# Performance work log

Measured on AMD Instinct MI355X. Metric: run time of the kernel, lower is better.

Reference implementation:

```python
import jax, jax.numpy as jnp
import numpy as np

VOCAB, D, H, L, T1, B = 32000, 1024, 1024, 2, 513, 64


def setup_inputs() -> dict:
    key = jax.random.key(0)
    ks = jax.random.split(key, 6)
    s = 1.0 / np.sqrt(H)
    return {
        "tokens": jax.random.randint(ks[0], (T1, B), 0, VOCAB),
        "emb": jax.random.normal(ks[1], (VOCAB, D), jnp.float32),
        "W_ih": jax.random.normal(ks[2], (L, 4 * H, D), jnp.float32) * s,
        "W_hh": jax.random.normal(ks[3], (L, 4 * H, H), jnp.float32) * s,
        "b_ih": jax.random.normal(ks[4], (L, 4 * H), jnp.float32) * s,
        "b_hh": jax.random.normal(ks[5], (L, 4 * H), jnp.float32) * s,
    }


def _lstm_cell(x, h, c, W_ih_l, W_hh_l, b_ih_l, b_hh_l):
    # gates: [B, 4H]; PyTorch LSTMCell gate order: i, f, g, o
    gates = x @ W_ih_l.T + b_ih_l + h @ W_hh_l.T + b_hh_l
    i, f, g, o = jnp.split(gates, 4, axis=-1)
    c_new = jax.nn.sigmoid(f) * c + jax.nn.sigmoid(i) * jnp.tanh(g)
    h_new = jax.nn.sigmoid(o) * jnp.tanh(c_new)
    return h_new, c_new


def reference(tokens, emb, W_ih, W_hh, b_ih, b_hh):
    ids = tokens[:-1]                       # [T, B] per `input[:-1]`
    emb_tab = emb.at[0].set(0.0)            # padding_idx = PAD = 0
    x = emb_tab[ids]                        # [T, B, D]

    h0 = jnp.zeros((L, x.shape[1], H), x.dtype)
    c0 = jnp.zeros((L, x.shape[1], H), x.dtype)

    def step(carry, x_t):
        h, c = carry                        # each [L, B, H]
        inp = x_t
        hs, cs = [], []
        for l in range(L):                  # L is small & static
            h_l, c_l = _lstm_cell(inp, h[l], c[l], W_ih[l], W_hh[l], b_ih[l], b_hh[l])
            inp = h_l                       # dropout=0.0 (eval): identity
            hs.append(h_l)
            cs.append(c_l)
        return (jnp.stack(hs), jnp.stack(cs)), inp

    _, outputs = jax.lax.scan(step, (h0, c0), x)
    return outputs                          # [T, B, H]
```

## Files before the change

### kernel.cpp

```cpp
#include <hip/hip_runtime.h>

typedef _Float16 half_t;
typedef _Float16 half8 __attribute__((ext_vector_type(8)));
typedef float floatx4 __attribute__((ext_vector_type(4)));
typedef int int4v __attribute__((ext_vector_type(4)));
typedef unsigned uint4v __attribute__((ext_vector_type(4)));
typedef unsigned char uchar;

#define NSTEP 512
#define INV2048 (1.0f / 2048.0f)
#define NSLOT 64
#define SLOTE 65536

__device__ __forceinline__ uchar enc_e5m2(float x) {
  half_t h = (half_t)x;
  unsigned b = (unsigned)__builtin_bit_cast(unsigned short, h);
  return (uchar)(((b + 0x80u) >> 8) & 0xffu);
}

__device__ __forceinline__ half8 dec8(unsigned w0, unsigned w1) {
  uint4v u;
  u[0] = ((w0 & 0x000000ffu) << 8) | ((w0 & 0x0000ff00u) << 16);
  u[1] = ((w0 & 0x00ff0000u) >> 8) | (w0 & 0xff000000u);
  u[2] = ((w1 & 0x000000ffu) << 8) | ((w1 & 0x0000ff00u) << 16);
  u[3] = ((w1 & 0x00ff0000u) >> 8) | (w1 & 0xff000000u);
  return __builtin_bit_cast(half8, u);
}

__global__ void conv_w(const float* __restrict__ Wih, const float* __restrict__ Whh,
                       half_t* __restrict__ whi, uchar* __restrict__ wlo) {
  long e = (long)blockIdx.x * 256 + threadIdx.x;
  int i    = (int)(e & 7);
  int lane = (int)((e >> 3) & 63);
  int frag = (int)((e >> 9) & 15);
  int wv   = (int)((e >> 13) & 7);
  int wg   = (int)((e >> 16) & 127);
  int layer = (int)((e >> 23) & 1);
  int mt = frag & 1, kk = (frag >> 1) & 3, prt = frag >> 3;
  int mloc = mt * 16 + (lane & 15);
  int grow = (mloc >> 3) * 1024 + wg * 8 + (mloc & 7);
  int k = prt * 1024 + wv * 128 + kk * 32 + ((lane >> 4) * 8) + i;
  long base = ((long)layer << 22) + (long)grow * 1024;
  float v = (k < 1024) ? Wih[base + k] : Whh[base + (k - 1024)];
  half_t hi = (half_t)v;
  whi[e] = hi;
  wlo[e] = enc_e5m2((v - (float)hi) * 2048.0f);
}

__device__ __forceinline__ float sigm(float x) { return 1.f / (1.f + __expf(-x)); }
__device__ __forceinline__ float tanh_f(float x) {
  x = fminf(15.f, fmaxf(-15.f, x));
  float e = __expf(-2.f * x);
  return (1.f - e) / (1.f + e);
}

__device__ __forceinline__ void pollcnt(const int* base, int n, int lane) {
  const int* p0 = base + lane;
  const int* p1 = base + 64 + lane;
  for (;;) {
    int v0 = __hip_atomic_load(p0, __ATOMIC_RELAXED, __HIP_MEMORY_SCOPE_AGENT);
    int v1 = __hip_atomic_load(p1, __ATOMIC_RELAXED, __HIP_MEMORY_SCOPE_AGENT);
    if (__all((v0 >= n) && (v1 >= n))) break;
    __builtin_amdgcn_s_sleep(2);
  }
}

__launch_bounds__(512, 1)
__global__ void lstm_main(const int* __restrict__ tokens, const float* __restrict__ emb,
                          const float* __restrict__ bih, const float* __restrict__ bhh,
                          const half_t* __restrict__ whi, const uchar* __restrict__ wlo,
                          half_t* __restrict__ h1h, half_t* __restrict__ h2h,
                          int* __restrict__ fc, float* __restrict__ out) {
  __shared__ float part[8][32][68];
  __shared__ volatile int gate0, gate1;
  const int wgid = blockIdx.x;
  const int layer = wgid >> 7;
  const int wg = wgid & 127;
  const int tid = (int)threadIdx.x;
  const int wv = tid >> 6;
  const int lane = tid & 63;
  const int ln15 = lane & 15;
  const int kr = (lane >> 4) * 8;

  const int* f0 = fc;
  const int* f1 = fc + 1024;

  half8 whi_r[16];
  {
    const half_t* wb = whi + (((long)(layer * 128 + wg)) << 16) + wv * 8192;
    #pragma unroll
    for (int f = 0; f < 16; ++f)
      whi_r[f] = *(const half8*)(wb + f * 512 + lane * 8);
  }
  unsigned lw[16][2];
  {
    const uchar* lobw = wlo + (((long)(layer * 128 + wg)) << 16) + wv * 8192;
    #pragma unroll
    for (int f = 0; f < 16; ++f) {
      const unsigned* l = (const unsigned*)(lobw + (f << 9) + lane * 8);
      lw[f][0] = l[0]; lw[f][1] = l[1];
    }
  }

  float bsum[4];
  {
    int u = tid & 7;
    for (int g = 0; g < 4; ++g) {
      int bi = layer * 4096 + g * 1024 + wg * 8 + u;
      bsum[g] = bih[bi] + bhh[bi];
    }
  }
  float c = 0.f;
  if (tid == 0) { gate0 = 0; gate1 = 0; }
  __syncthreads();

  for (int t = 0; t < NSTEP; ++t) {
    if (layer == 0) {
      if (wv == 0 && t > 0) {
        pollcnt(f0, t, lane);
        if (t >= 49) pollcnt(f1, t - 48, lane);
        if (lane == 0) gate1 = t;
      }
    } else {
      if (wv == 0) {
        pollcnt(f0, t + 1, lane);
        if (lane == 0) gate0 = t + 1;
      } else if (wv == 1 && t > 0) {
        pollcnt(f1, t, lane);
        if (lane == 0) gate1 = t;
      }
    }

    floatx4 zero = {0.f, 0.f, 0.f, 0.f};
    floatx4 acc_h[2][4], acc_l[2][4];
    for (int a = 0; a < 2; ++a)
      for (int b = 0; b < 4; ++b) { acc_h[a][b] = zero; acc_l[a][b] = zero; }

    if (layer == 0) {
      int tk[4]; const float* rowp[4]; float msk[4];
      #pragma unroll
      for (int nt = 0; nt < 4; ++nt) {
        tk[nt] = tokens[t * 64 + nt * 16 + ln15];
        rowp[nt] = emb + (long)tk[nt] * 1024;
        msk[nt] = (tk[nt] == 0) ? 0.f : 1.f;
      }
      floatx4 bx0[2][4], bx1[2][4];
      {
        int kb = wv * 128 + kr;
        #pragma unroll
        for (int nt = 0; nt < 4; ++nt) {
          bx0[0][nt] = *(const floatx4*)(rowp[nt] + kb);
          bx1[0][nt] = *(const floatx4*)(rowp[nt] + kb + 4);
        }
      }
      #pragma unroll
      for (int kk = 0; kk < 4; ++kk) {
        const int cb = kk & 1, nx = cb ^ 1;
        if (kk < 3) {
          int kb = wv * 128 + (kk + 1) * 32 + kr;
          #pragma unroll
          for (int nt = 0; nt < 4; ++nt) {
            bx0[nx][nt] = *(const floatx4*)(rowp[nt] + kb);
            bx1[nx][nt] = *(const floatx4*)(rowp[nt] + kb + 4);
          }
        }
        half8 ah0 = whi_r[kk * 2];
        half8 ah1 = whi_r[kk * 2 + 1];
        half8 al0 = dec8(lw[kk * 2][0], lw[kk * 2][1]);
        half8 al1 = dec8(lw[kk * 2 + 1][0], lw[kk * 2 + 1][1]);
        #pragma unroll
        for (int nt = 0; nt < 4; ++nt) {
          half8 bh;
          #pragma unroll
          for (int q = 0; q < 4; ++q) {
            bh[q]     = (half_t)(bx0[cb][nt][q] * msk[nt]);
            bh[q + 4] = (half_t)(bx1[cb][nt][q] * msk[nt]);
          }
          acc_h[0][nt] = __builtin_amdgcn_mfma_f32_16x16x32_f16(ah0, bh, acc_h[0][nt], 0, 0, 0);
          acc_h[1][nt] = __builtin_amdgcn_mfma_f32_16x16x32_f16(ah1, bh, acc_h[1][nt], 0, 0, 0);
          acc_l[0][nt] = __builtin_amdgcn_mfma_f32_16x16x32_f16(al0, bh, acc_l[0][nt], 0, 0, 0);
          acc_l[1][nt] = __builtin_amdgcn_mfma_f32_16x16x32_f16(al1, bh, acc_l[1][nt], 0, 0, 0);
        }
      }
    } else {
      while (gate0 < t + 1) __builtin_amdgcn_s_sleep(1);
      const half_t* abh = h1h + (long)(t & (NSLOT - 1)) * SLOTE;
      const int kofs = wv * 128;
      half8 bufh[4][4];
      #pragma unroll
      for (int kk = 0; kk < 4; ++kk) {
        int kb = kofs + kk * 32 + kr;
        #pragma unroll
        for (int nt = 0; nt < 4; ++nt)
          bufh[kk][nt] = *(const half8*)(abh + (nt * 16 + ln15) * 1024 + kb);
      }
      #pragma unroll
      for (int kk = 0; kk < 4; ++kk) {
        half8 ah0 = whi_r[kk * 2];
        half8 ah1 = whi_r[kk * 2 + 1];
        half8 al0 = dec8(lw[kk * 2][0], lw[kk * 2][1]);
        half8 al1 = dec8(lw[kk * 2 + 1][0], lw[kk * 2 + 1][1]);
        #pragma unroll
        for (int nt = 0; nt < 4; ++nt) {
          half8 bh = bufh[kk][nt];
          acc_h[0][nt] = __builtin_amdgcn_mfma_f32_16x16x32_f16(ah0, bh, acc_h[0][nt], 0, 0, 0);
          acc_h[1][nt] = __builtin_amdgcn_mfma_f32_16x16x32_f16(ah1, bh, acc_h[1][nt], 0, 0, 0);
          acc_l[0][nt] = __builtin_amdgcn_mfma_f32_16x16x32_f16(al0, bh, acc_l[0][nt], 0, 0, 0);
          acc_l[1][nt] = __builtin_amdgcn_mfma_f32_16x16x32_f16(al1, bh, acc_l[1][nt], 0, 0, 0);
        }
      }
    }

    if (t > 0) {
      while (gate1 < t) __builtin_amdgcn_s_sleep(1);
      const half_t* abh = (layer == 0 ? h1h : h2h) + (long)((t - 1) & (NSLOT - 1)) * SLOTE;
      const int kofs = wv * 128;
      half8 bufh[4][4];
      #pragma unroll
      for (int kk = 0; kk < 4; ++kk) {
        int kb = kofs + kk * 32 + kr;
        #pragma unroll
        for (int nt = 0; nt < 4; ++nt)
          bufh[kk][nt] = *(const half8*)(abh + (nt * 16 + ln15) * 1024 + kb);
      }
      #pragma unroll
      for (int kk = 0; kk < 4; ++kk) {
        half8 ah0 = whi_r[8 + kk * 2];
        half8 ah1 = whi_r[8 + kk * 2 + 1];
        half8 al0 = dec8(lw[8 + kk * 2][0], lw[8 + kk * 2][1]);
        half8 al1 = dec8(lw[8 + kk * 2 + 1][0], lw[8 + kk * 2 + 1][1]);
        #pragma unroll
        for (int nt = 0; nt < 4; ++nt) {
          half8 bh = bufh[kk][nt];
          acc_h[0][nt] = __builtin_amdgcn_mfma_f32_16x16x32_f16(ah0, bh, acc_h[0][nt], 0, 0, 0);
          acc_h[1][nt] = __builtin_amdgcn_mfma_f32_16x16x32_f16(ah1, bh, acc_h[1][nt], 0, 0, 0);
          acc_l[0][nt] = __builtin_amdgcn_mfma_f32_16x16x32_f16(al0, bh, acc_l[0][nt], 0, 0, 0);
          acc_l[1][nt] = __builtin_amdgcn_mfma_f32_16x16x32_f16(al1, bh, acc_l[1][nt], 0, 0, 0);
        }
      }
    }

    #pragma unroll
    for (int mt = 0; mt < 2; ++mt)
      #pragma unroll
      for (int nt = 0; nt < 4; ++nt)
        #pragma unroll
        for (int q = 0; q < 4; ++q)
          part[wv][mt * 16 + (lane >> 4) * 4 + q][nt * 16 + ln15] =
              acc_h[mt][nt][q] + INV2048 * acc_l[mt][nt][q];
    __syncthreads();
    float hkeep;
    {
      int u = tid & 7, n = tid >> 3;
      float s0 = bsum[0], s1 = bsum[1], s2 = bsum[2], s3 = bsum[3];
      #pragma unroll
      for (int w = 0; w < 8; ++w) {
        s0 += part[w][u][n];
        s1 += part[w][8 + u][n];
        s2 += part[w][16 + u][n];
        s3 += part[w][24 + u][n];
      }
      float is = sigm(s0), fs = sigm(s1), gt = tanh_f(s2), os = sigm(s3);
      c = fs * c + is * gt;
      hkeep = os * tanh_f(c);
      half_t hhi = (half_t)hkeep;
      half_t* hb = (layer == 0 ? h1h : h2h) + (long)(t & (NSLOT - 1)) * SLOTE;
      __hip_atomic_store((unsigned short*)&hb[n * 1024 + wg * 8 + u],
                         __builtin_bit_cast(unsigned short, hhi),
                         __ATOMIC_RELAXED, __HIP_MEMORY_SCOPE_AGENT);
    }
    __syncthreads();
    if (tid == 0) {
      asm volatile("s_waitcnt vmcnt(0)" ::: "memory");
      __hip_atomic_store(fc + layer * 1024 + wg, t + 1,
                         __ATOMIC_RELAXED, __HIP_MEMORY_SCOPE_AGENT);
    }
    if (layer == 1) {
      int u = tid & 7, n = tid >> 3;
      __builtin_nontemporal_store(hkeep, &out[((long)t * 64 + n) * 1024 + wg * 8 + u]);
    }
    if ((t & 31) == 31)
      __builtin_amdgcn_fence(__ATOMIC_ACQUIRE, "agent");
  }
}

extern "C" void kernel_launch(void* const* d_in, const int* in_sizes, int n_in,
                              void* d_out, int out_size, void* d_ws, size_t ws_size,
                              hipStream_t stream) {
  const int*   tokens = (const int*)d_in[0];
  const float* emb    = (const float*)d_in[1];
  const float* Wih    = (const float*)d_in[2];
  const float* Whh    = (const float*)d_in[3];
  const float* bih    = (const float*)d_in[4];
  const float* bhh    = (const float*)d_in[5];
  float* out = (float*)d_out;

  half_t* whi = (half_t*)d_ws;
  uchar*  wlo = (uchar*)((char*)d_ws + 33554432);
  half_t* h1h = (half_t*)((char*)d_ws + 50331648);
  half_t* h2h = (half_t*)((char*)d_ws + 58720256);
  int* fc     = (int*)((char*)d_ws + 67108864);

  hipLaunchKernelGGL(conv_w, dim3(65536), dim3(256), 0, stream, Wih, Whh, whi, wlo);
  hipMemsetAsync(fc, 0, 8192, stream);

  void* args[] = {(void*)&tokens, (void*)&emb, (void*)&bih, (void*)&bhh,
                  (void*)&whi, (void*)&wlo, (void*)&h1h, (void*)&h2h,
                  (void*)&fc, (void*)&out};
  hipError_t e = hipLaunchCooperativeKernel((const void*)lstm_main, dim3(256), dim3(512),
                                            args, 0, stream);
  if (e != hipSuccess) {
    hipMemsetAsync(d_out, 0x43, (size_t)out_size * 4, stream);
  }
}
```

Measured before the change: 7.843 ms.

## Decentralize per-wave flag polling, pad flags, double-buffer partials and drop a barrier

Each wave now polls only the 16 producer flags covering its own K slice instead of wave 0 polling every flag and releasing the block through LDS gates. Flags are padded to separate 256-byte lines. The partial-sum LDS buffer is double-buffered, which lets the trailing __syncthreads be replaced by an LDS atomic counter whose last arriving wave publishes the completion flag. The aim is to cut the inter-workgroup synchronization latency on the recurrent critical path. In exchange, ordering now rests on per-wave waitcnt and relaxed atomics, and the layer-1 backpressure check on layer 0 runs only every 16 steps.

```diff
diff --git a/kernel.cpp b/kernel.cpp
--- a/kernel.cpp
+++ b/kernel.cpp
@@ -11,6 +11,7 @@
 #define INV2048 (1.0f / 2048.0f)
 #define NSLOT 64
 #define SLOTE 65536
+#define FSTRIDE 64
 
 __device__ __forceinline__ uchar enc_e5m2(float x) {
   half_t h = (half_t)x;
@@ -54,9 +55,15 @@
   return (1.f - e) / (1.f + e);
 }
 
-__device__ __forceinline__ void pollcnt(const int* base, int n, int lane) {
-  const int* p0 = base + lane;
-  const int* p1 = base + 64 + lane;
+__device__ __forceinline__ void pollN(const int* fbase, int first, int n, int lane) {
+  const int* p = fbase + (first + (lane & 15)) * FSTRIDE;
+  while (__hip_atomic_load(p, __ATOMIC_RELAXED, __HIP_MEMORY_SCOPE_AGENT) < n)
+    __builtin_amdgcn_s_sleep(2);
+}
+
+__device__ __forceinline__ void pollFull(const int* fbase, int n, int lane) {
+  const int* p0 = fbase + lane * FSTRIDE;
+  const int* p1 = fbase + (64 + lane) * FSTRIDE;
   for (;;) {
     int v0 = __hip_atomic_load(p0, __ATOMIC_RELAXED, __HIP_MEMORY_SCOPE_AGENT);
     int v1 = __hip_atomic_load(p1, __ATOMIC_RELAXED, __HIP_MEMORY_SCOPE_AGENT);
@@ -71,8 +78,8 @@
                           const half_t* __restrict__ whi, const uchar* __restrict__ wlo,
                           half_t* __restrict__ h1h, half_t* __restrict__ h2h,
                           int* __restrict__ fc, float* __restrict__ out) {
-  __shared__ float part[8][32][68];
-  __shared__ volatile int gate0, gate1;
+  __shared__ float part[2][8][32][68];
+  __shared__ int dcnt;
   const int wgid = blockIdx.x;
   const int layer = wgid >> 7;
   const int wg = wgid & 127;
@@ -83,7 +90,7 @@
   const int kr = (lane >> 4) * 8;
 
   const int* f0 = fc;
-  const int* f1 = fc + 1024;
+  const int* f1 = fc + 128 * FSTRIDE;
 
   half8 whi_r[16];
   {
@@ -111,24 +118,19 @@
     }
   }
   float c = 0.f;
-  if (tid == 0) { gate0 = 0; gate1 = 0; }
+  if (tid == 0) dcnt = 0;
   __syncthreads();
 
   for (int t = 0; t < NSTEP; ++t) {
     if (layer == 0) {
-      if (wv == 0 && t > 0) {
-        pollcnt(f0, t, lane);
-        if (t >= 49) pollcnt(f1, t - 48, lane);
-        if (lane == 0) gate1 = t;
-      }
+      if ((t & 15) == 0 && t >= 33) pollFull(f1, t - 32, lane);
+      if (t > 0) pollN(f0, wv * 16, t, lane);
     } else {
-      if (wv == 0) {
-        pollcnt(f0, t + 1, lane);
-        if (lane == 0) gate0 = t + 1;
-      } else if (wv == 1 && t > 0) {
-        pollcnt(f1, t, lane);
-        if (lane == 0) gate1 = t;
-      }
+      const int sel = (lane >> 4) & 1;
+      const int* p = (sel ? f0 : f1) + (wv * 16 + ln15) * FSTRIDE;
+      const int thr = sel ? (t + 1) : t;
+      while (__hip_atomic_load(p, __ATOMIC_RELAXED, __HIP_MEMORY_SCOPE_AGENT) < thr)
+        __builtin_amdgcn_s_sleep(2);
     }
 
     floatx4 zero = {0.f, 0.f, 0.f, 0.f};
@@ -183,7 +185,6 @@
         }
       }
     } else {
-      while (gate0 < t + 1) __builtin_amdgcn_s_sleep(1);
       const half_t* abh = h1h + (long)(t & (NSLOT - 1)) * SLOTE;
       const int kofs = wv * 128;
       half8 bufh[4][4];
@@ -212,7 +213,6 @@
     }
 
     if (t > 0) {
-      while (gate1 < t) __builtin_amdgcn_s_sleep(1);
       const half_t* abh = (layer == 0 ? h1h : h2h) + (long)((t - 1) & (NSLOT - 1)) * SLOTE;
       const int kofs = wv * 128;
       half8 bufh[4][4];
@@ -240,13 +240,14 @@
       }
     }
 
+    const int pb = t & 1;
     #pragma unroll
     for (int mt = 0; mt < 2; ++mt)
       #pragma unroll
       for (int nt = 0; nt < 4; ++nt)
         #pragma unroll
         for (int q = 0; q < 4; ++q)
-          part[wv][mt * 16 + (lane >> 4) * 4 + q][nt * 16 + ln15] =
+          part[pb][wv][mt * 16 + (lane >> 4) * 4 + q][nt * 16 + ln15] =
               acc_h[mt][nt][q] + INV2048 * acc_l[mt][nt][q];
     __syncthreads();
     float hkeep;
@@ -255,10 +256,10 @@
       float s0 = bsum[0], s1 = bsum[1], s2 = bsum[2], s3 = bsum[3];
       #pragma unroll
       for (int w = 0; w < 8; ++w) {
-        s0 += part[w][u][n];
-        s1 += part[w][8 + u][n];
-        s2 += part[w][16 + u][n];
-        s3 += part[w][24 + u][n];
+        s0 += part[pb][w][u][n];
+        s1 += part[pb][w][8 + u][n];
+        s2 += part[pb][w][16 + u][n];
+        s3 += part[pb][w][24 + u][n];
       }
       float is = sigm(s0), fs = sigm(s1), gt = tanh_f(s2), os = sigm(s3);
       c = fs * c + is * gt;
@@ -269,11 +270,12 @@
                          __builtin_bit_cast(unsigned short, hhi),
                          __ATOMIC_RELAXED, __HIP_MEMORY_SCOPE_AGENT);
     }
-    __syncthreads();
-    if (tid == 0) {
-      asm volatile("s_waitcnt vmcnt(0)" ::: "memory");
-      __hip_atomic_store(fc + layer * 1024 + wg, t + 1,
-                         __ATOMIC_RELAXED, __HIP_MEMORY_SCOPE_AGENT);
+    asm volatile("s_waitcnt vmcnt(0)" ::: "memory");
+    if (lane == 0) {
+      int old = atomicAdd(&dcnt, 1);
+      if (old == t * 8 + 7)
+        __hip_atomic_store(fc + (layer * 128 + wg) * FSTRIDE, t + 1,
+                           __ATOMIC_RELAXED, __HIP_MEMORY_SCOPE_AGENT);
     }
     if (layer == 1) {
       int u = tid & 7, n = tid >> 3;
@@ -302,7 +304,7 @@
   int* fc     = (int*)((char*)d_ws + 67108864);
 
   hipLaunchKernelGGL(conv_w, dim3(65536), dim3(256), 0, stream, Wih, Whh, whi, wlo);
-  hipMemsetAsync(fc, 0, 8192, stream);
+  hipMemsetAsync(fc, 0, 65536, stream);
 
   void* args[] = {(void*)&tokens, (void*)&emb, (void*)&bih, (void*)&bhh,
                   (void*)&whi, (void*)&wlo, (void*)&h1h, (void*)&h2h,
```

New measurement: 7.671 ms. -2.2%, faster.
